# Kernel optimization log

Hardware: AMD Instinct MI355X
Metric: run time of the kernel (lower is better)

Reference implementation:

```python
import jax, jax.numpy as jnp
import numpy as np

B, T, D, H = 2, 2048, 1024, 16
STD = 0.02

def setup_inputs() -> dict:
    key = jax.random.key(0)
    ks = jax.random.split(key, 5)
    x = jax.random.normal(ks[0], (B, T, D), dtype=jnp.float32)
    Wq = jax.random.normal(ks[1], (D, D), dtype=jnp.float32) * STD
    Wk = jax.random.normal(ks[2], (D, D), dtype=jnp.float32) * STD
    Wv = jax.random.normal(ks[3], (D, D), dtype=jnp.float32) * STD
    Wo = jax.random.normal(ks[4], (D, D), dtype=jnp.float32) * STD
    z = jnp.zeros((D,), dtype=jnp.float32)
    return {"x": x, "Wq": Wq, "bq": z, "Wk": Wk, "bk": z, "Wv": Wv, "bv": z, "Wo": Wo, "bo": z}

def _split(t, h):
    b, s, dm = t.shape
    return t.reshape(b, s, h, dm // h).transpose(0, 2, 1, 3)  # (B,h,T,d)

def reference(x, Wq, bq, Wk, bk, Wv, bv, Wo, bo):
    h = H
    # linear projections (nn.Linear: y = x @ W^T + b)
    q = _split(x @ Wq.T + bq, h)
    k = _split(x @ Wk.T + bk, h)
    v = _split(x @ Wv.T + bv, h)
    d_k = k.shape[-1]
    # scaled dot-product similarities (B,h,T,T)
    sim = jnp.einsum("bhqd,bhkd->bhqk", q, k) / jnp.sqrt(jnp.float32(d_k))
    # causal mask: upper triangle (excluding diag) filled with -inf
    Tq = sim.shape[-1]
    causal = jnp.tril(jnp.ones((Tq, Tq), dtype=bool))
    sim = jnp.where(causal, sim, -jnp.inf)
    attn = jax.nn.softmax(sim, axis=-1)
    ctx = jnp.einsum("bhqk,bhkd->bhqd", attn, v)  # (B,h,T,d)
    ctx = ctx.transpose(0, 2, 1, 3).reshape(x.shape[0], x.shape[1], -1)  # (B,T,D)
    return ctx @ Wo.T + bo
```

## Files before the change

### kernel.cpp

```cpp
#include <hip/hip_runtime.h>
#include <hip/hip_bf16.h>


typedef __attribute__((ext_vector_type(8))) short bf16x8;
typedef __attribute__((ext_vector_type(4))) float f32x4;
typedef __attribute__((ext_vector_type(4))) short s16x4;

#define QSCALE 0.18033688011f

__device__ __forceinline__ int sniff_f32(const void* p) {
    const unsigned short* u = (const unsigned short*)p;
    int c = 0;
    for (int i = 0; i < 256; ++i) {
        int e = (u[i] >> 7) & 0xFF;
        c += (e >= 0x90) ? 1 : 0;
    }
    return c > 8;
}

__device__ __forceinline__ void async_copy16(const void* g, void* l) {
    __builtin_amdgcn_global_load_lds(
        (const __attribute__((address_space(1))) void*)g,
        (__attribute__((address_space(3))) void*)l, 16, 0, 0);
}

struct Cvt { const void* src; __hip_bfloat16* dst; int n; };
struct CvtPack { Cvt a[9]; };

__global__ __launch_bounds__(256) void cvt_bf16(CvtPack pk) {
    const Cvt c = pk.a[blockIdx.y];
    const int f32 = sniff_f32(c.src);
    const int stride = gridDim.x * 256 * 8;
    for (int idx = (blockIdx.x * 256 + threadIdx.x) * 8; idx < c.n; idx += stride) {
        if (f32) {
            const float* s = (const float*)c.src + idx;
            f32x4 a0 = *(const f32x4*)s;
            f32x4 a1 = *(const f32x4*)(s + 4);
            union { __hip_bfloat16 h[8]; bf16x8 v; } u;
#pragma unroll
            for (int e = 0; e < 4; e++) u.h[e]     = (__hip_bfloat16)a0[e];
#pragma unroll
            for (int e = 0; e < 4; e++) u.h[4 + e] = (__hip_bfloat16)a1[e];
            *(bf16x8*)&c.dst[idx] = u.v;
        } else {
            *(bf16x8*)&c.dst[idx] = *(const bf16x8*)((const __hip_bfloat16*)c.src + idx);
        }
    }
}

template <int MODE>
__device__ __forceinline__ void gemm_async_body(
    const __hip_bfloat16* __restrict__ A, const __hip_bfloat16* __restrict__ W,
    const __hip_bfloat16* __restrict__ bias, void* __restrict__ C,
    int M, int N, int K, int bm, int bn, float outscale,
    __hip_bfloat16* smem)
{
    const int tid  = threadIdx.x;
    const int wave = tid >> 6;
    const int lane = tid & 63;
    const int quad = lane >> 4;
    const int l15  = lane & 15;
    const int wr   = wave >> 1;
    const int wc   = wave & 1;

    const int srow = wave * 16 + (lane >> 2);
    const int scol = (lane & 3) * 8;
    const __hip_bfloat16* gA0 = A + (size_t)(bm + srow) * K + scol;
    const __hip_bfloat16* gB0 = W + (size_t)(bn + srow) * K + scol;

    f32x4 acc[4][4];
#pragma unroll
    for (int i = 0; i < 4; i++)
#pragma unroll
        for (int j = 0; j < 4; j++) acc[i][j] = (f32x4)0.0f;

#define QSTAGE(buf, k0) { \
        __hip_bfloat16* d_ = smem + (buf) * 8192 + wave * 512; \
        async_copy16(gA0 + (k0), d_); \
        async_copy16(gA0 + (size_t)64 * K + (k0), d_ + 2048); \
        async_copy16(gB0 + (k0), d_ + 4096); \
        async_copy16(gB0 + (size_t)64 * K + (k0), d_ + 4096 + 2048); \
    }

    const int nt = K >> 5;
    QSTAGE(0, 0);
    for (int t = 0; t < nt; ++t) {
        const int buf = t & 1;
        const __hip_bfloat16* sA = smem + buf * 8192;
        const __hip_bfloat16* sB = sA + 4096;
        if (t + 1 < nt) {
            QSTAGE(1 - buf, (t + 1) * 32);
            asm volatile("s_waitcnt vmcnt(4)" ::: "memory");
        } else {
            asm volatile("s_waitcnt vmcnt(0)" ::: "memory");
        }
        __builtin_amdgcn_s_barrier();

        bf16x8 af[4], bf[4];
#pragma unroll
        for (int i = 0; i < 4; i++)
            af[i] = *(const bf16x8*)&sA[(wr * 64 + i * 16 + l15) * 32 + quad * 8];
#pragma unroll
        for (int j = 0; j < 4; j++)
            bf[j] = *(const bf16x8*)&sB[(wc * 64 + j * 16 + l15) * 32 + quad * 8];
#pragma unroll
        for (int i = 0; i < 4; i++)
#pragma unroll
            for (int j = 0; j < 4; j++)
                acc[i][j] = __builtin_amdgcn_mfma_f32_16x16x32_bf16(af[i], bf[j], acc[i][j], 0, 0, 0);

        __builtin_amdgcn_s_barrier();
    }
#undef QSTAGE

    float bv[4];
#pragma unroll
    for (int j = 0; j < 4; j++)
        bv[j] = (float)bias[bn + wc * 64 + j * 16 + l15];

    if (MODE == 2) {
        __hip_bfloat16* sOut = smem;
        __syncthreads();
#pragma unroll
        for (int i = 0; i < 4; i++) {
            int tl = wr * 64 + i * 16 + quad * 4;
#pragma unroll
            for (int j = 0; j < 4; j++) {
                int dl = wc * 64 + j * 16 + l15;
                union { __hip_bfloat16 e[4]; s16x4 v; } u;
#pragma unroll
                for (int r = 0; r < 4; r++)
                    u.e[r] = (__hip_bfloat16)(acc[i][j][r] + bv[j]);
                *(s16x4*)&sOut[dl * 136 + tl] = u.v;
            }
        }
        __syncthreads();
        __hip_bfloat16* VTo = (__hip_bfloat16*)C;
        const int bb = bm >> 11, tt0 = bm & 2047;
#pragma unroll
        for (int g8 = 0; g8 < 8; g8++) {
            int idx = g8 * 256 + tid;
            int dl  = idx >> 4;
            int tc  = (idx & 15) * 8;
            int dg  = bn + dl;
            bf16x8 v = *(const bf16x8*)&sOut[dl * 136 + tc];
            *(bf16x8*)&VTo[(((size_t)bb * 16 + (dg >> 6)) * 64 + (dg & 63)) * 2048 + tt0 + tc] = v;
        }
    } else {
#pragma unroll
        for (int i = 0; i < 4; i++) {
#pragma unroll
            for (int j = 0; j < 4; j++) {
                int col = bn + wc * 64 + j * 16 + l15;
#pragma unroll
                for (int r = 0; r < 4; r++) {
                    int row = bm + wr * 64 + i * 16 + quad * 4 + r;
                    float v = (acc[i][j][r] + bv[j]) * outscale;
                    if (MODE == 1) ((float*)C)[(size_t)row * N + col] = v;
                    else ((__hip_bfloat16*)C)[(size_t)row * N + col] = (__hip_bfloat16)v;
                }
            }
        }
    }
}

__global__ __launch_bounds__(256, 2) void qkv_gemm(
    const __hip_bfloat16* __restrict__ x,
    const __hip_bfloat16* __restrict__ Wq, const __hip_bfloat16* __restrict__ bq, __hip_bfloat16* __restrict__ Q,
    const __hip_bfloat16* __restrict__ Wk, const __hip_bfloat16* __restrict__ bk, __hip_bfloat16* __restrict__ Kb,
    const __hip_bfloat16* __restrict__ Wv, const __hip_bfloat16* __restrict__ bv, __hip_bfloat16* __restrict__ VT,
    int M, int N, int K)
{
    __shared__ __hip_bfloat16 smem[128 * 136];
    if (blockIdx.z == 0)
        gemm_async_body<0>(x, Wq, bq, Q, M, N, K, blockIdx.x * 128, blockIdx.y * 128, QSCALE, smem);
    else if (blockIdx.z == 1)
        gemm_async_body<0>(x, Wk, bk, Kb, M, N, K, blockIdx.x * 128, blockIdx.y * 128, 1.0f, smem);
    else
        gemm_async_body<2>(x, Wv, bv, VT, M, N, K, blockIdx.x * 128, blockIdx.y * 128, 1.0f, smem);
}

template <bool OF32>
__device__ __forceinline__ void gemm64_body(
    const __hip_bfloat16* __restrict__ A, const __hip_bfloat16* __restrict__ W,
    const __hip_bfloat16* __restrict__ bias, void* __restrict__ C,
    int M, int N, int K, int bm, int bn,
    __hip_bfloat16* smem)
{
    const int tid  = threadIdx.x;
    const int wave = tid >> 6;
    const int lane = tid & 63;
    const int quad = lane >> 4;
    const int l15  = lane & 15;

    const int srow = wave * 16 + (lane >> 2);
    const int scol = (lane & 3) * 8;
    const __hip_bfloat16* gA0 = A + (size_t)(bm + srow) * K + scol;
    const __hip_bfloat16* gB0 = W + (size_t)(bn + srow) * K + scol;

    f32x4 acc[4][2];
#pragma unroll
    for (int i = 0; i < 4; i++)
#pragma unroll
        for (int j = 0; j < 2; j++) acc[i][j] = (f32x4)0.0f;

#define OSTAGE(buf, k0) { \
        __hip_bfloat16* d_ = smem + (buf) * 6144; \
        async_copy16(gA0 + (k0), d_ + wave * 512); \
        async_copy16(gB0 + (k0), d_ + 2048 + wave * 512); \
        async_copy16(gB0 + (size_t)64 * K + (k0), d_ + 2048 + wave * 512 + 2048); \
    }

    const int nt = K >> 5;
    OSTAGE(0, 0);
    for (int t = 0; t < nt; ++t) {
        const int buf = t & 1;
        const __hip_bfloat16* sA = smem + buf * 6144;
        const __hip_bfloat16* sB = sA + 2048;
        if (t + 1 < nt) {
            OSTAGE(1 - buf, (t + 1) * 32);
            asm volatile("s_waitcnt vmcnt(3)" ::: "memory");
        } else {
            asm volatile("s_waitcnt vmcnt(0)" ::: "memory");
        }
        __builtin_amdgcn_s_barrier();

        bf16x8 af[4], bf[2];
#pragma unroll
        for (int i = 0; i < 4; i++)
            af[i] = *(const bf16x8*)&sA[(i * 16 + l15) * 32 + quad * 8];
#pragma unroll
        for (int j = 0; j < 2; j++)
            bf[j] = *(const bf16x8*)&sB[(wave * 32 + j * 16 + l15) * 32 + quad * 8];
#pragma unroll
        for (int i = 0; i < 4; i++)
#pragma unroll
            for (int j = 0; j < 2; j++)
                acc[i][j] = __builtin_amdgcn_mfma_f32_16x16x32_bf16(af[i], bf[j], acc[i][j], 0, 0, 0);

        __builtin_amdgcn_s_barrier();
    }
#undef OSTAGE

    float bv[2];
#pragma unroll
    for (int j = 0; j < 2; j++)
        bv[j] = (float)bias[bn + wave * 32 + j * 16 + l15];
#pragma unroll
    for (int i = 0; i < 4; i++) {
#pragma unroll
        for (int j = 0; j < 2; j++) {
            int col = bn + wave * 32 + j * 16 + l15;
#pragma unroll
            for (int r = 0; r < 4; r++) {
                int row = bm + i * 16 + quad * 4 + r;
                float v = acc[i][j][r] + bv[j];
                if (OF32) ((float*)C)[(size_t)row * N + col] = v;
                else      ((__hip_bfloat16*)C)[(size_t)row * N + col] = (__hip_bfloat16)v;
            }
        }
    }
}

__global__ __launch_bounds__(256, 2) void out_gemm(
    const __hip_bfloat16* __restrict__ A, const __hip_bfloat16* __restrict__ W,
    const __hip_bfloat16* __restrict__ bias, const void* __restrict__ origW,
    void* __restrict__ C, int M, int N, int K)
{
    __shared__ __hip_bfloat16 smem[2 * 6144];
    __shared__ int f32flag;
    if (threadIdx.x == 0) f32flag = sniff_f32(origW);
    __syncthreads();
    if (f32flag)
        gemm64_body<true>(A, W, bias, C, M, N, K, blockIdx.x * 64, blockIdx.y * 128, smem);
    else
        gemm64_body<false>(A, W, bias, C, M, N, K, blockIdx.x * 64, blockIdx.y * 128, smem);
}

#define PAD 68

__global__ __launch_bounds__(512, 4) void attn_causal(
    const __hip_bfloat16* __restrict__ Q,
    const __hip_bfloat16* __restrict__ K,
    const __hip_bfloat16* __restrict__ VT,
    __hip_bfloat16* __restrict__ O,
    int T, int D, int H)
{
    __shared__ __hip_bfloat16 sK[2][64 * PAD];
    __shared__ __hip_bfloat16 sVT[2][64 * PAD];
    __shared__ __hip_bfloat16 sPA[8][16 * PAD];

    const int tid  = threadIdx.x;
    const int wave = tid >> 6;
    const int lane = tid & 63;
    const int quad = lane >> 4;
    const int l15  = lane & 15;

    const int NT = T >> 7;
    const int qt = blockIdx.z ? (NT - 1 - (int)blockIdx.x) : (int)blockIdx.x;
    const int h  = blockIdx.y;
    const int b  = blockIdx.z;
    const size_t headoff = (size_t)b * T * D + (size_t)h * 64;
    const size_t vtoff   = ((size_t)b * H + h) * 64 * (size_t)T;

    const int nkt = 2 * qt + 2;
    const int qbase    = qt * 128 + wave * 16;
    const int myrowmax = qbase + 15;

    bf16x8 qfrag[2];
#pragma unroll
    for (int kk = 0; kk < 2; kk++)
        qfrag[kk] = *(const bf16x8*)&Q[headoff +
            (size_t)(qbase + l15) * D + kk * 32 + quad * 8];

    f32x4 acc_o[4];
#pragma unroll
    for (int j = 0; j < 4; j++) acc_o[j] = (f32x4)0.0f;
    float lacc = 0.f;

    const int srow = tid >> 3;
    const int sc8  = (tid & 7) * 8;

    bf16x8 pk, pv;
    pk = *(const bf16x8*)&K[headoff + (size_t)srow * D + sc8];
    pv = *(const bf16x8*)&VT[vtoff + (size_t)srow * T + sc8];
    *(bf16x8*)&sK[0][srow * PAD + sc8]  = pk;
    *(bf16x8*)&sVT[0][srow * PAD + sc8] = pv;
    if (nkt > 1) {
        pk = *(const bf16x8*)&K[headoff + (size_t)(64 + srow) * D + sc8];
        pv = *(const bf16x8*)&VT[vtoff + (size_t)srow * T + 64 + sc8];
    }
    __syncthreads();

    for (int kt = 0; kt < nkt; ++kt) {
        const int cur = kt & 1;

        if (kt + 1 < nkt) {
            *(bf16x8*)&sK[1 - cur][srow * PAD + sc8]  = pk;
            *(bf16x8*)&sVT[1 - cur][srow * PAD + sc8] = pv;
            if (kt + 2 < nkt) {
                pk = *(const bf16x8*)&K[headoff + (size_t)((kt + 2) * 64 + srow) * D + sc8];
                pv = *(const bf16x8*)&VT[vtoff + (size_t)srow * T + (kt + 2) * 64 + sc8];
            }
        }

        if (kt * 64 <= myrowmax) {
            bf16x8 kfrag[2][4], vfrag[2][4];
#pragma unroll
            for (int kk = 0; kk < 2; kk++)
#pragma unroll
                for (int j = 0; j < 4; j++) {
                    kfrag[kk][j] = *(const bf16x8*)&sK[cur][(j * 16 + l15) * PAD + kk * 32 + quad * 8];
                    vfrag[kk][j] = *(const bf16x8*)&sVT[cur][(j * 16 + l15) * PAD + kk * 32 + quad * 8];
                }

            f32x4 st[4];
#pragma unroll
            for (int j = 0; j < 4; j++) st[j] = (f32x4)0.0f;
            __builtin_amdgcn_s_setprio(1);
#pragma unroll
            for (int kk = 0; kk < 2; kk++)
#pragma unroll
                for (int j = 0; j < 4; j++)
                    st[j] = __builtin_amdgcn_mfma_f32_16x16x32_bf16(
                        kfrag[kk][j], qfrag[kk], st[j], 0, 0, 0);
            __builtin_amdgcn_s_setprio(0);

            if (kt * 64 + 63 > qbase) {
                const int q = qbase + l15;
#pragma unroll
                for (int j = 0; j < 4; j++) {
                    int keyb = kt * 64 + j * 16 + quad * 4;
#pragma unroll
                    for (int r = 0; r < 4; r++)
                        if (keyb + r > q) st[j][r] = -1e30f;
                }
            }

#pragma unroll
            for (int j = 0; j < 4; j++) {
                union { __hip_bfloat16 e[4]; s16x4 v; } u;
#pragma unroll
                for (int r = 0; r < 4; r++) {
                    float p = exp2f(st[j][r]);
                    lacc += p;
                    u.e[r] = (__hip_bfloat16)p;
                }
                *(s16x4*)&sPA[wave][l15 * PAD + j * 16 + quad * 4] = u.v;
            }
            __builtin_amdgcn_s_setprio(1);
#pragma unroll
            for (int kk = 0; kk < 2; kk++) {
                bf16x8 a = *(const bf16x8*)&sPA[wave][l15 * PAD + kk * 32 + quad * 8];
#pragma unroll
                for (int j = 0; j < 4; j++)
                    acc_o[j] = __builtin_amdgcn_mfma_f32_16x16x32_bf16(
                        a, vfrag[kk][j], acc_o[j], 0, 0, 0);
            }
            __builtin_amdgcn_s_setprio(0);
        }

        __syncthreads();
    }

    lacc += __shfl_xor(lacc, 16, 64);
    lacc += __shfl_xor(lacc, 32, 64);

#pragma unroll
    for (int r = 0; r < 4; r++) {
        float linv = 1.0f / __shfl(lacc, quad * 4 + r, 64);
        int row = qbase + quad * 4 + r;
#pragma unroll
        for (int j = 0; j < 4; j++) {
            int col = j * 16 + l15;
            O[headoff + (size_t)row * D + col] = (__hip_bfloat16)(acc_o[j][r] * linv);
        }
    }
}

extern "C" void kernel_launch(void* const* d_in, const int* in_sizes, int n_in,
                              void* d_out, int out_size, void* d_ws, size_t ws_size,
                              hipStream_t stream) {
    const int Bb = 2, T = 2048, D = 1024, H = 16;
    const int M = Bb * T;

    __hip_bfloat16* w = (__hip_bfloat16*)d_ws;
    __hip_bfloat16* Q   = w;
    __hip_bfloat16* Kb  = Q   + (size_t)M * D;
    __hip_bfloat16* VT  = Kb  + (size_t)M * D;
    __hip_bfloat16* ctx = VT  + (size_t)M * D;
    __hip_bfloat16* xb  = ctx + (size_t)M * D;
    __hip_bfloat16* Wqb = xb  + (size_t)M * D;
    __hip_bfloat16* Wkb = Wqb + (size_t)D * D;
    __hip_bfloat16* Wvb = Wkb + (size_t)D * D;
    __hip_bfloat16* Wob = Wvb + (size_t)D * D;
    __hip_bfloat16* bqb = Wob + (size_t)D * D;
    __hip_bfloat16* bkb = bqb + D;
    __hip_bfloat16* bvb = bkb + D;
    __hip_bfloat16* bob = bvb + D;

    CvtPack pk;
    pk.a[0] = { d_in[0], xb,  M * D };
    pk.a[1] = { d_in[1], Wqb, D * D };
    pk.a[2] = { d_in[2], bqb, D };
    pk.a[3] = { d_in[3], Wkb, D * D };
    pk.a[4] = { d_in[4], bkb, D };
    pk.a[5] = { d_in[5], Wvb, D * D };
    pk.a[6] = { d_in[6], bvb, D };
    pk.a[7] = { d_in[7], Wob, D * D };
    pk.a[8] = { d_in[8], bob, D };

    cvt_bf16<<<dim3(512, 9), 256, 0, stream>>>(pk);
    qkv_gemm<<<dim3(M / 128, D / 128, 3), 256, 0, stream>>>(
        xb, Wqb, bqb, Q, Wkb, bkb, Kb, Wvb, bvb, VT, M, D, D);
    attn_causal<<<dim3(T / 128, H, Bb), 512, 0, stream>>>(Q, Kb, VT, ctx, T, D, H);
    out_gemm<<<dim3(M / 64, D / 128), 256, 0, stream>>>(
        ctx, Wob, bob, d_in[7], d_out, M, D, D);
}
```

Measured before the change: 206.8 us.

## Split longest causal attention tiles across two blocks with combine pass

The four longest query tiles (qt 12-15) of each head are split in half along the key dimension, and a static schedule table orders blocks so long work starts first. Split halves write unnormalized fp32 partial outputs and row sums into reused workspace, and a new combine kernel merges and normalizes them. This targets tail imbalance from causal masking at the cost of an extra launch, extra global traffic, and a lowered occupancy hint. The merge skips any max rescaling, which is valid only if the softmax uses no per-block running max.

After: 211.3 us. 1.02x slower.

```diff
diff --git a/kernel.cpp b/kernel.cpp
--- a/kernel.cpp
+++ b/kernel.cpp
@@ -7,6 +7,9 @@
 typedef __attribute__((ext_vector_type(4))) short s16x4;
 
 #define QSCALE 0.18033688011f
+
+__constant__ int QTA[20] = {11,10,9,8,15,15,7,14,14,13,13,6,12,12,5,4,3,2,1,0};
+__constant__ int HFA[20] = {-1,-1,-1,-1,0,1,-1,0,1,0,1,-1,0,1,-1,-1,-1,-1,-1,-1};
 
 __device__ __forceinline__ int sniff_f32(const void* p) {
     const unsigned short* u = (const unsigned short*)p;
@@ -279,11 +282,12 @@
 
 #define PAD 68
 
-__global__ __launch_bounds__(512, 4) void attn_causal(
+__global__ __launch_bounds__(512, 2) void attn_causal(
     const __hip_bfloat16* __restrict__ Q,
     const __hip_bfloat16* __restrict__ K,
     const __hip_bfloat16* __restrict__ VT,
     __hip_bfloat16* __restrict__ O,
+    float* __restrict__ PO, float* __restrict__ PL,
     int T, int D, int H)
 {
     __shared__ __hip_bfloat16 sK[2][64 * PAD];
@@ -296,14 +300,22 @@
     const int quad = lane >> 4;
     const int l15  = lane & 15;
 
-    const int NT = T >> 7;
-    const int qt = blockIdx.z ? (NT - 1 - (int)blockIdx.x) : (int)blockIdx.x;
-    const int h  = blockIdx.y;
-    const int b  = blockIdx.z;
+    const int srow = tid >> 3;
+    const int sc8  = (tid & 7) * 8;
+
+    const int rank = blockIdx.x >> 5;
+    const int hb   = blockIdx.x & 31;
+    const int h    = hb & 15;
+    const int b    = hb >> 4;
+    const int qt   = QTA[rank];
+    const int hf   = HFA[rank];
+    const int nkt  = 2 * qt + 2;
+    const int mid  = qt + 1;
+    const int kt0  = (hf == 1) ? mid : 0;
+    const int kt1  = (hf == 0) ? mid : nkt;
+
     const size_t headoff = (size_t)b * T * D + (size_t)h * 64;
     const size_t vtoff   = ((size_t)b * H + h) * 64 * (size_t)T;
-
-    const int nkt = 2 * qt + 2;
     const int qbase    = qt * 128 + wave * 16;
     const int myrowmax = qbase + 15;
 
@@ -318,27 +330,24 @@
     for (int j = 0; j < 4; j++) acc_o[j] = (f32x4)0.0f;
     float lacc = 0.f;
 
-    const int srow = tid >> 3;
-    const int sc8  = (tid & 7) * 8;
-
     bf16x8 pk, pv;
-    pk = *(const bf16x8*)&K[headoff + (size_t)srow * D + sc8];
-    pv = *(const bf16x8*)&VT[vtoff + (size_t)srow * T + sc8];
+    pk = *(const bf16x8*)&K[headoff + (size_t)(kt0 * 64 + srow) * D + sc8];
+    pv = *(const bf16x8*)&VT[vtoff + (size_t)srow * T + kt0 * 64 + sc8];
     *(bf16x8*)&sK[0][srow * PAD + sc8]  = pk;
     *(bf16x8*)&sVT[0][srow * PAD + sc8] = pv;
-    if (nkt > 1) {
-        pk = *(const bf16x8*)&K[headoff + (size_t)(64 + srow) * D + sc8];
-        pv = *(const bf16x8*)&VT[vtoff + (size_t)srow * T + 64 + sc8];
+    if (kt0 + 1 < kt1) {
+        pk = *(const bf16x8*)&K[headoff + (size_t)((kt0 + 1) * 64 + srow) * D + sc8];
+        pv = *(const bf16x8*)&VT[vtoff + (size_t)srow * T + (kt0 + 1) * 64 + sc8];
     }
     __syncthreads();
 
-    for (int kt = 0; kt < nkt; ++kt) {
-        const int cur = kt & 1;
-
-        if (kt + 1 < nkt) {
+    for (int kt = kt0; kt < kt1; ++kt) {
+        const int cur = (kt - kt0) & 1;
+
+        if (kt + 1 < kt1) {
             *(bf16x8*)&sK[1 - cur][srow * PAD + sc8]  = pk;
             *(bf16x8*)&sVT[1 - cur][srow * PAD + sc8] = pv;
-            if (kt + 2 < nkt) {
+            if (kt + 2 < kt1) {
                 pk = *(const bf16x8*)&K[headoff + (size_t)((kt + 2) * 64 + srow) * D + sc8];
                 pv = *(const bf16x8*)&VT[vtoff + (size_t)srow * T + (kt + 2) * 64 + sc8];
             }
@@ -406,15 +415,51 @@
     lacc += __shfl_xor(lacc, 16, 64);
     lacc += __shfl_xor(lacc, 32, 64);
 
-#pragma unroll
-    for (int r = 0; r < 4; r++) {
-        float linv = 1.0f / __shfl(lacc, quad * 4 + r, 64);
-        int row = qbase + quad * 4 + r;
-#pragma unroll
-        for (int j = 0; j < 4; j++) {
-            int col = j * 16 + l15;
-            O[headoff + (size_t)row * D + col] = (__hip_bfloat16)(acc_o[j][r] * linv);
-        }
+    if (hf >= 0) {
+        const int pidx = (((b * 16 + h) * 4) + (qt - 12)) * 2 + hf;
+        float* POt = PO + (size_t)pidx * 8192;
+#pragma unroll
+        for (int r = 0; r < 4; r++) {
+            int rl = wave * 16 + quad * 4 + r;
+#pragma unroll
+            for (int j = 0; j < 4; j++)
+                POt[rl * 64 + j * 16 + l15] = acc_o[j][r];
+        }
+        if (quad == 0) PL[pidx * 128 + wave * 16 + l15] = lacc;
+    } else {
+#pragma unroll
+        for (int r = 0; r < 4; r++) {
+            float linv = 1.0f / __shfl(lacc, quad * 4 + r, 64);
+            int row = qbase + quad * 4 + r;
+#pragma unroll
+            for (int j = 0; j < 4; j++) {
+                int col = j * 16 + l15;
+                O[headoff + (size_t)row * D + col] = (__hip_bfloat16)(acc_o[j][r] * linv);
+            }
+        }
+    }
+}
+
+__global__ __launch_bounds__(256) void attn_combine(
+    const float* __restrict__ PO, const float* __restrict__ PL,
+    __hip_bfloat16* __restrict__ O, int T, int D, int H)
+{
+    const int tix = blockIdx.x;
+    const int qt  = 12 + (tix & 3);
+    const int h   = (tix >> 2) & 15;
+    const int b   = tix >> 6;
+    const float* P0 = PO + (size_t)(2 * tix) * 8192;
+    const float* P1 = P0 + 8192;
+    const float* L0 = PL + 2 * tix * 128;
+    const float* L1 = L0 + 128;
+    const size_t headoff = (size_t)b * T * D + (size_t)h * 64;
+    const int rowbase = qt * 128;
+
+    for (int e = threadIdx.x; e < 8192; e += 256) {
+        int rr = e >> 6, cc = e & 63;
+        float linv = 1.0f / (L0[rr] + L1[rr]);
+        float v = (P0[e] + P1[e]) * linv;
+        O[headoff + (size_t)(rowbase + rr) * D + cc] = (__hip_bfloat16)v;
     }
 }
 
@@ -439,6 +484,9 @@
     __hip_bfloat16* bvb = bkb + D;
     __hip_bfloat16* bob = bvb + D;
 
+    float* PO = (float*)xb;
+    float* PL = (float*)Wqb;
+
     CvtPack pk;
     pk.a[0] = { d_in[0], xb,  M * D };
     pk.a[1] = { d_in[1], Wqb, D * D };
@@ -453,7 +501,9 @@
     cvt_bf16<<<dim3(512, 9), 256, 0, stream>>>(pk);
     qkv_gemm<<<dim3(M / 128, D / 128, 3), 256, 0, stream>>>(
         xb, Wqb, bqb, Q, Wkb, bkb, Kb, Wvb, bvb, VT, M, D, D);
-    attn_causal<<<dim3(T / 128, H, Bb), 512, 0, stream>>>(Q, Kb, VT, ctx, T, D, H);
+    attn_causal<<<dim3(640, 1, 1), 512, 0, stream>>>(
+        Q, Kb, VT, ctx, PO, PL, T, D, H);
+    attn_combine<<<dim3(128, 1, 1), 256, 0, stream>>>(PO, PL, ctx, T, D, H);
     out_gemm<<<dim3(M / 64, D / 128), 256, 0, stream>>>(
         ctx, Wob, bob, d_in[7], d_out, M, D, D);
 }
```

## Process 32 query rows per wave to double K/V tile reuse in causal attention

Applied to the files above, without the earlier changes.

Each wave of the attention kernel now handles two 16-row query groups instead of one, so each block covers 256 query rows and the grid along T is halved. Every K/V tile staged in LDS and loaded into registers is reused by twice as many MFMAs, which halves global K/V traffic per query. The cost is higher register and LDS use (the P buffer doubles), only 256 blocks in the grid, and coarser causal tiles that do more wasted work on the diagonal and balance load less evenly.

After: 375.6 us. 1.82x slower.

```diff
diff --git a/kernel.cpp b/kernel.cpp
--- a/kernel.cpp
+++ b/kernel.cpp
@@ -288,7 +288,7 @@
 {
     __shared__ __hip_bfloat16 sK[2][64 * PAD];
     __shared__ __hip_bfloat16 sVT[2][64 * PAD];
-    __shared__ __hip_bfloat16 sPA[8][16 * PAD];
+    __shared__ __hip_bfloat16 sPA[8][32 * PAD];
 
     const int tid  = threadIdx.x;
     const int wave = tid >> 6;
@@ -296,27 +296,31 @@
     const int quad = lane >> 4;
     const int l15  = lane & 15;
 
-    const int NT = T >> 7;
+    const int NT = T >> 8;
     const int qt = blockIdx.z ? (NT - 1 - (int)blockIdx.x) : (int)blockIdx.x;
     const int h  = blockIdx.y;
     const int b  = blockIdx.z;
     const size_t headoff = (size_t)b * T * D + (size_t)h * 64;
     const size_t vtoff   = ((size_t)b * H + h) * 64 * (size_t)T;
 
-    const int nkt = 2 * qt + 2;
-    const int qbase    = qt * 128 + wave * 16;
-    const int myrowmax = qbase + 15;
-
-    bf16x8 qfrag[2];
-#pragma unroll
-    for (int kk = 0; kk < 2; kk++)
-        qfrag[kk] = *(const bf16x8*)&Q[headoff +
-            (size_t)(qbase + l15) * D + kk * 32 + quad * 8];
-
-    f32x4 acc_o[4];
-#pragma unroll
-    for (int j = 0; j < 4; j++) acc_o[j] = (f32x4)0.0f;
-    float lacc = 0.f;
+    const int nkt = 4 * qt + 4;
+    const int qbase    = qt * 256 + wave * 32;
+    const int myrowmax = qbase + 31;
+
+    bf16x8 qfrag[2][2];
+#pragma unroll
+    for (int g = 0; g < 2; g++)
+#pragma unroll
+        for (int kk = 0; kk < 2; kk++)
+            qfrag[g][kk] = *(const bf16x8*)&Q[headoff +
+                (size_t)(qbase + g * 16 + l15) * D + kk * 32 + quad * 8];
+
+    f32x4 acc_o[2][4];
+#pragma unroll
+    for (int g = 0; g < 2; g++)
+#pragma unroll
+        for (int j = 0; j < 4; j++) acc_o[g][j] = (f32x4)0.0f;
+    float lacc[2] = {0.f, 0.f};
 
     const int srow = tid >> 3;
     const int sc8  = (tid & 7) * 8;
@@ -354,68 +358,79 @@
                     vfrag[kk][j] = *(const bf16x8*)&sVT[cur][(j * 16 + l15) * PAD + kk * 32 + quad * 8];
                 }
 
-            f32x4 st[4];
-#pragma unroll
-            for (int j = 0; j < 4; j++) st[j] = (f32x4)0.0f;
+#pragma unroll
+            for (int g = 0; g < 2; g++) {
+                const int qb = qbase + g * 16;
+                f32x4 st[4];
+#pragma unroll
+                for (int j = 0; j < 4; j++) st[j] = (f32x4)0.0f;
+                __builtin_amdgcn_s_setprio(1);
+#pragma unroll
+                for (int kk = 0; kk < 2; kk++)
+#pragma unroll
+                    for (int j = 0; j < 4; j++)
+                        st[j] = __builtin_amdgcn_mfma_f32_16x16x32_bf16(
+                            kfrag[kk][j], qfrag[g][kk], st[j], 0, 0, 0);
+                __builtin_amdgcn_s_setprio(0);
+
+                if (kt * 64 + 63 > qb) {
+                    const int q = qb + l15;
+#pragma unroll
+                    for (int j = 0; j < 4; j++) {
+                        int keyb = kt * 64 + j * 16 + quad * 4;
+#pragma unroll
+                        for (int r = 0; r < 4; r++)
+                            if (keyb + r > q) st[j][r] = -1e30f;
+                    }
+                }
+
+#pragma unroll
+                for (int j = 0; j < 4; j++) {
+                    union { __hip_bfloat16 e[4]; s16x4 v; } u;
+#pragma unroll
+                    for (int r = 0; r < 4; r++) {
+                        float p = exp2f(st[j][r]);
+                        lacc[g] += p;
+                        u.e[r] = (__hip_bfloat16)p;
+                    }
+                    *(s16x4*)&sPA[wave][(g * 16 + l15) * PAD + j * 16 + quad * 4] = u.v;
+                }
+            }
             __builtin_amdgcn_s_setprio(1);
 #pragma unroll
-            for (int kk = 0; kk < 2; kk++)
-#pragma unroll
-                for (int j = 0; j < 4; j++)
-                    st[j] = __builtin_amdgcn_mfma_f32_16x16x32_bf16(
-                        kfrag[kk][j], qfrag[kk], st[j], 0, 0, 0);
+            for (int g = 0; g < 2; g++)
+#pragma unroll
+                for (int kk = 0; kk < 2; kk++) {
+                    bf16x8 a = *(const bf16x8*)&sPA[wave][(g * 16 + l15) * PAD + kk * 32 + quad * 8];
+#pragma unroll
+                    for (int j = 0; j < 4; j++)
+                        acc_o[g][j] = __builtin_amdgcn_mfma_f32_16x16x32_bf16(
+                            a, vfrag[kk][j], acc_o[g][j], 0, 0, 0);
+                }
             __builtin_amdgcn_s_setprio(0);
-
-            if (kt * 64 + 63 > qbase) {
-                const int q = qbase + l15;
-#pragma unroll
-                for (int j = 0; j < 4; j++) {
-                    int keyb = kt * 64 + j * 16 + quad * 4;
-#pragma unroll
-                    for (int r = 0; r < 4; r++)
-                        if (keyb + r > q) st[j][r] = -1e30f;
-                }
-            }
-
+        }
+
+        __syncthreads();
+    }
+
+#pragma unroll
+    for (int g = 0; g < 2; g++) {
+        lacc[g] += __shfl_xor(lacc[g], 16, 64);
+        lacc[g] += __shfl_xor(lacc[g], 32, 64);
+    }
+
+#pragma unroll
+    for (int g = 0; g < 2; g++)
+#pragma unroll
+        for (int r = 0; r < 4; r++) {
+            float linv = 1.0f / __shfl(lacc[g], quad * 4 + r, 64);
+            int row = qbase + g * 16 + quad * 4 + r;
 #pragma unroll
             for (int j = 0; j < 4; j++) {
-                union { __hip_bfloat16 e[4]; s16x4 v; } u;
-#pragma unroll
-                for (int r = 0; r < 4; r++) {
-                    float p = exp2f(st[j][r]);
-                    lacc += p;
-                    u.e[r] = (__hip_bfloat16)p;
-                }
-                *(s16x4*)&sPA[wave][l15 * PAD + j * 16 + quad * 4] = u.v;
-            }
-            __builtin_amdgcn_s_setprio(1);
-#pragma unroll
-            for (int kk = 0; kk < 2; kk++) {
-                bf16x8 a = *(const bf16x8*)&sPA[wave][l15 * PAD + kk * 32 + quad * 8];
-#pragma unroll
-                for (int j = 0; j < 4; j++)
-                    acc_o[j] = __builtin_amdgcn_mfma_f32_16x16x32_bf16(
-                        a, vfrag[kk][j], acc_o[j], 0, 0, 0);
-            }
-            __builtin_amdgcn_s_setprio(0);
-        }
-
-        __syncthreads();
-    }
-
-    lacc += __shfl_xor(lacc, 16, 64);
-    lacc += __shfl_xor(lacc, 32, 64);
-
-#pragma unroll
-    for (int r = 0; r < 4; r++) {
-        float linv = 1.0f / __shfl(lacc, quad * 4 + r, 64);
-        int row = qbase + quad * 4 + r;
-#pragma unroll
-        for (int j = 0; j < 4; j++) {
-            int col = j * 16 + l15;
-            O[headoff + (size_t)row * D + col] = (__hip_bfloat16)(acc_o[j][r] * linv);
-        }
-    }
+                int col = j * 16 + l15;
+                O[headoff + (size_t)row * D + col] = (__hip_bfloat16)(acc_o[g][j][r] * linv);
+            }
+        }
 }
 
 extern "C" void kernel_launch(void* const* d_in, const int* in_sizes, int n_in,
@@ -453,7 +468,7 @@
     cvt_bf16<<<dim3(512, 9), 256, 0, stream>>>(pk);
     qkv_gemm<<<dim3(M / 128, D / 128, 3), 256, 0, stream>>>(
         xb, Wqb, bqb, Q, Wkb, bkb, Kb, Wvb, bvb, VT, M, D, D);
-    attn_causal<<<dim3(T / 128, H, Bb), 512, 0, stream>>>(Q, Kb, VT, ctx, T, D, H);
+    attn_causal<<<dim3(T / 256, H, Bb), 512, 0, stream>>>(Q, Kb, VT, ctx, T, D, H);
     out_gemm<<<dim3(M / 64, D / 128), 256, 0, stream>>>(
         ctx, Wob, bob, d_in[7], d_out, M, D, D);
 }
```
